# Kernel tuning notes

Hardware: AMD Instinct MI355X
Metric: run time of the kernel (lower is better)

Reference implementation:

```python
import jax, jax.numpy as jnp
import numpy as np

N, F_IN, H, C, E = 100000, 128, 64, 40, 1600000
NEG_SLOPE = 0.2


def setup_inputs() -> dict:
    key = jax.random.key(0)
    ks = jax.random.split(key, 12)
    s = 0.1
    return {
        "x": jax.random.normal(ks[0], (N, F_IN), jnp.float32),
        "edge_index": jax.random.randint(ks[1], (2, E), 0, N, jnp.int32),
        "W1": jax.random.normal(ks[2], (F_IN, H), jnp.float32) * s,
        "a_src1": jax.random.normal(ks[3], (H,), jnp.float32) * s,
        "a_dst1": jax.random.normal(ks[4], (H,), jnp.float32) * s,
        "b1": jnp.zeros((H,), jnp.float32),
        "W2": jax.random.normal(ks[5], (H, H), jnp.float32) * s,
        "a_src2": jax.random.normal(ks[6], (H,), jnp.float32) * s,
        "a_dst2": jax.random.normal(ks[7], (H,), jnp.float32) * s,
        "b2": jnp.zeros((H,), jnp.float32),
        "Wl": jax.random.normal(ks[8], (H, C), jnp.float32) * s,
        "bl": jnp.zeros((C,), jnp.float32),
    }


def gat_conv(x, src, dst, W, a_src, a_dst, b):
    # PyG GATConv, heads=1, self-loops already appended to (src, dst)
    h = x @ W                                   # [N, H]
    alpha_s = h @ a_src                         # [N]
    alpha_d = h @ a_dst                         # [N]
    e = jax.nn.leaky_relu(alpha_s[src] + alpha_d[dst], NEG_SLOPE)  # [E]
    # segment softmax over incoming edges of each target node
    m = jax.ops.segment_max(e, dst, num_segments=x.shape[0])
    ex = jnp.exp(e - m[dst])
    denom = jax.ops.segment_sum(ex, dst, num_segments=x.shape[0])
    w = ex / (denom[dst] + 1e-16)               # [E]
    out = jax.ops.segment_sum(h[src] * w[:, None], dst, num_segments=x.shape[0])
    return out + b


def reference(x, edge_index, W1, a_src1, a_dst1, b1, W2, a_src2, a_dst2, b2, Wl, bl):
    n = x.shape[0]
    loops = jnp.arange(n, dtype=edge_index.dtype)
    src = jnp.concatenate([edge_index[0], loops])
    dst = jnp.concatenate([edge_index[1], loops])
    h = gat_conv(x, src, dst, W1, a_src1, a_dst1, b1)
    h = jax.nn.relu(h)  # dropout p=0 -> identity
    h = gat_conv(h, src, dst, W2, a_src2, a_dst2, b2)
    logits = h @ Wl + bl
    return jax.nn.log_softmax(logits, axis=-1)
```

## Files before the change

kernel.cpp:

```cpp
#include <hip/hip_runtime.h>
#include <math.h>


#define NEG_SLOPE 0.2f
#define NEG_BIG -3.0e38f

#define BSHIFT 9
#define BSIZE 512
#define BCAP 12288
#define EPB 4096

typedef __bf16 bf16x8 __attribute__((ext_vector_type(8)));
typedef __bf16 bf16x4 __attribute__((ext_vector_type(4)));
typedef float f32x4 __attribute__((ext_vector_type(4)));

__device__ __forceinline__ float lrelu(float x) {
    return x >= 0.f ? x : NEG_SLOPE * x;
}

__device__ __forceinline__ int wave_incl_scan(int v, int lane) {
#pragma unroll
    for (int d = 1; d < 64; d <<= 1) {
        int t = __shfl_up(v, d, 64);
        if (lane >= d) v += t;
    }
    return v;
}


__global__ __launch_bounds__(256) void fused_scatter_gemm(
        const int* __restrict__ src, const int* __restrict__ dst,
        int* __restrict__ bucketCount, unsigned* __restrict__ ebuf, int E, int SB,
        const float* __restrict__ X, const float* __restrict__ W,
        const float* __restrict__ a_src, const float* __restrict__ a_dst,
        __bf16* __restrict__ Hout, float* __restrict__ as_, float* __restrict__ ad_,
        int N, int nTiles) {
    constexpr int K = 128;
    __shared__ __bf16 Whi[64][K + 8];
    __shared__ __bf16 Wlo[64][K + 8];
    __shared__ int hist[256], base[256];

    if (blockIdx.x < (unsigned)SB) {
        const int t = threadIdx.x;
        hist[t] = 0;
        __syncthreads();
        const int e0 = blockIdx.x * EPB;
        const int e1 = min(e0 + EPB, E);
        int rr[EPB / 256];
#pragma unroll
        for (int i = 0; i < EPB / 256; ++i) {
            int e = e0 + i * 256 + t;
            if (e < e1) rr[i] = atomicAdd(&hist[dst[e] >> BSHIFT], 1);
        }
        __syncthreads();
        if (hist[t] > 0) base[t] = atomicAdd(&bucketCount[t], hist[t]);
        __syncthreads();
#pragma unroll
        for (int i = 0; i < EPB / 256; ++i) {
            int e = e0 + i * 256 + t;
            if (e < e1) {
                int d = dst[e];
                int b = d >> BSHIFT;
                ebuf[(size_t)b * BCAP + base[b] + rr[i]] =
                    ((unsigned)src[e] << BSHIFT) | (unsigned)(d & (BSIZE - 1));
            }
        }
        return;
    }

    const int gbid = blockIdx.x - SB;
    for (int idx = threadIdx.x; idx < K * 64; idx += 256) {
        int k = idx >> 6, n = idx & 63;
        float w = W[idx];
        __bf16 hi = (__bf16)w;
        Whi[n][k] = hi;
        Wlo[n][k] = (__bf16)(w - (float)hi);
    }
    __syncthreads();

    const int lane  = threadIdx.x & 63;
    const int wave  = threadIdx.x >> 6;
    const int row16 = lane & 15;
    const int quad  = lane >> 4;

    float asv[4], adv[4];
#pragma unroll
    for (int t = 0; t < 4; ++t) {
        asv[t] = a_src[t * 16 + row16];
        adv[t] = a_dst[t * 16 + row16];
    }

    for (int tile = gbid; tile < nTiles; tile += 1024) {
        const int nbase = tile * 64;
        int gn = nbase + wave * 16 + row16;
        if (gn >= N) gn = N - 1;
        const float* __restrict__ xp = X + (size_t)gn * K + quad * 8;

        float4 xv[K / 16];
#pragma unroll
        for (int c = 0; c < K / 32; ++c) {
            xv[2 * c]     = *(const float4*)(xp + c * 32);
            xv[2 * c + 1] = *(const float4*)(xp + c * 32 + 4);
        }

        f32x4 acc[4] = {{0.f, 0.f, 0.f, 0.f}, {0.f, 0.f, 0.f, 0.f},
                        {0.f, 0.f, 0.f, 0.f}, {0.f, 0.f, 0.f, 0.f}};
#pragma unroll
        for (int kc = 0; kc < K; kc += 32) {
            float xs[8];
            *(float4*)&xs[0] = xv[kc / 16];
            *(float4*)&xs[4] = xv[kc / 16 + 1];
            bf16x8 ahi, alo;
#pragma unroll
            for (int j = 0; j < 8; ++j) {
                __bf16 hi = (__bf16)xs[j];
                ahi[j] = hi;
                alo[j] = (__bf16)(xs[j] - (float)hi);
            }
#pragma unroll
            for (int t = 0; t < 4; ++t) {
                bf16x8 bhi = *(const bf16x8*)&Whi[t * 16 + row16][kc + quad * 8];
                bf16x8 blo = *(const bf16x8*)&Wlo[t * 16 + row16][kc + quad * 8];
                acc[t] = __builtin_amdgcn_mfma_f32_16x16x32_bf16(ahi, bhi, acc[t], 0, 0, 0);
                acc[t] = __builtin_amdgcn_mfma_f32_16x16x32_bf16(ahi, blo, acc[t], 0, 0, 0);
                acc[t] = __builtin_amdgcn_mfma_f32_16x16x32_bf16(alo, bhi, acc[t], 0, 0, 0);
            }
        }

        float ps[4] = {0.f, 0.f, 0.f, 0.f};
        float pd[4] = {0.f, 0.f, 0.f, 0.f};
#pragma unroll
        for (int t = 0; t < 4; ++t) {
#pragma unroll
            for (int r = 0; r < 4; ++r) {
                int gm = nbase + wave * 16 + quad * 4 + r;
                if (gm < N) Hout[(size_t)gm * 64 + t * 16 + row16] = (__bf16)acc[t][r];
                ps[r] = fmaf(acc[t][r], asv[t], ps[r]);
                pd[r] = fmaf(acc[t][r], adv[t], pd[r]);
            }
        }
#pragma unroll
        for (int r = 0; r < 4; ++r) {
#pragma unroll
            for (int d = 1; d < 16; d <<= 1) {
                ps[r] += __shfl_xor(ps[r], d, 64);
                pd[r] += __shfl_xor(pd[r], d, 64);
            }
        }
        if (row16 == 0) {
#pragma unroll
            for (int r = 0; r < 4; ++r) {
                int gm = nbase + wave * 16 + quad * 4 + r;
                if (gm < N) { as_[gm] = ps[r]; ad_[gm] = pd[r]; }
            }
        }
    }
}


__global__ __launch_bounds__(512) void bucket_csr(const unsigned* __restrict__ ebuf,
                                                  const int* __restrict__ bucketCount,
                                                  int* __restrict__ offs,
                                                  int* __restrict__ csr, int N, int E) {
    __shared__ int hist[512], excls[512], wsum[8];
    const int b = blockIdx.x;
    const int t = threadIdx.x;
    const int lane = t & 63;
    const int w = t >> 6;

    int v = (t < 256 && t < b) ? bucketCount[t] : 0;
#pragma unroll
    for (int d = 32; d; d >>= 1) v += __shfl_xor(v, d, 64);
    if (lane == 0) wsum[w] = v;
    hist[t] = 0;
    __syncthreads();
    int gbase = 0;
#pragma unroll
    for (int i = 0; i < 8; ++i) gbase += wsum[i];
    const int cnt = bucketCount[b];
    if (b == 0 && t == 0) offs[N] = E;

    const unsigned* __restrict__ eb = ebuf + (size_t)b * BCAP;
    int rr[BCAP / 512];
#pragma unroll
    for (int i = 0; i < BCAP / 512; ++i) {
        int idx = i * 512 + t;
        if (idx < cnt) rr[i] = atomicAdd(&hist[eb[idx] & (BSIZE - 1)], 1);
    }
    __syncthreads();

    int hv = hist[t];
    int incl = wave_incl_scan(hv, lane);
    if (lane == 63) wsum[w] = incl;
    __syncthreads();
    int prefix = 0;
    for (int i = 0; i < 8; ++i) prefix += (i < w) ? wsum[i] : 0;
    int excl = incl - hv + prefix;
    int n = b * BSIZE + t;
    if (n < N) offs[n] = gbase + excl;
    excls[t] = excl;
    __syncthreads();

#pragma unroll
    for (int i = 0; i < BCAP / 512; ++i) {
        int idx = i * 512 + t;
        if (idx < cnt) {
            unsigned rec = eb[idx];
            csr[gbase + excls[rec & (BSIZE - 1)] + rr[i]] = (int)(rec >> BSHIFT);
        }
    }
}


__global__ __launch_bounds__(256) void gemm_mfma2(const __bf16* __restrict__ X,
                                                  const float* __restrict__ W,
                                                  const float* __restrict__ a_src,
                                                  const float* __restrict__ a_dst,
                                                  __bf16* __restrict__ Hout,
                                                  float* __restrict__ as_,
                                                  float* __restrict__ ad_,
                                                  int N, int nTiles) {
    constexpr int K = 64;
    __shared__ __bf16 Whi[64][K + 8];
    __shared__ __bf16 Wlo[64][K + 8];
    for (int idx = threadIdx.x; idx < K * 64; idx += 256) {
        int k = idx >> 6, n = idx & 63;
        float w = W[idx];
        __bf16 hi = (__bf16)w;
        Whi[n][k] = hi;
        Wlo[n][k] = (__bf16)(w - (float)hi);
    }
    __syncthreads();

    const int lane  = threadIdx.x & 63;
    const int wave  = threadIdx.x >> 6;
    const int row16 = lane & 15;
    const int quad  = lane >> 4;

    float asv[4], adv[4];
#pragma unroll
    for (int t = 0; t < 4; ++t) {
        asv[t] = a_src[t * 16 + row16];
        adv[t] = a_dst[t * 16 + row16];
    }

    for (int tile = blockIdx.x; tile < nTiles; tile += gridDim.x) {
        const int nbase = tile * 64;
        int gn = nbase + wave * 16 + row16;
        if (gn >= N) gn = N - 1;
        const __bf16* __restrict__ xp = X + (size_t)gn * K + quad * 8;
        bf16x8 a0 = *(const bf16x8*)(xp);
        bf16x8 a1 = *(const bf16x8*)(xp + 32);

        f32x4 acc[4] = {{0.f, 0.f, 0.f, 0.f}, {0.f, 0.f, 0.f, 0.f},
                        {0.f, 0.f, 0.f, 0.f}, {0.f, 0.f, 0.f, 0.f}};
#pragma unroll
        for (int kc = 0; kc < K; kc += 32) {
            bf16x8 a = (kc == 0) ? a0 : a1;
#pragma unroll
            for (int t = 0; t < 4; ++t) {
                bf16x8 bhi = *(const bf16x8*)&Whi[t * 16 + row16][kc + quad * 8];
                bf16x8 blo = *(const bf16x8*)&Wlo[t * 16 + row16][kc + quad * 8];
                acc[t] = __builtin_amdgcn_mfma_f32_16x16x32_bf16(a, bhi, acc[t], 0, 0, 0);
                acc[t] = __builtin_amdgcn_mfma_f32_16x16x32_bf16(a, blo, acc[t], 0, 0, 0);
            }
        }

        float ps[4] = {0.f, 0.f, 0.f, 0.f};
        float pd[4] = {0.f, 0.f, 0.f, 0.f};
#pragma unroll
        for (int t = 0; t < 4; ++t) {
#pragma unroll
            for (int r = 0; r < 4; ++r) {
                int gm = nbase + wave * 16 + quad * 4 + r;
                if (gm < N) Hout[(size_t)gm * 64 + t * 16 + row16] = (__bf16)acc[t][r];
                ps[r] = fmaf(acc[t][r], asv[t], ps[r]);
                pd[r] = fmaf(acc[t][r], adv[t], pd[r]);
            }
        }
#pragma unroll
        for (int r = 0; r < 4; ++r) {
#pragma unroll
            for (int d = 1; d < 16; d <<= 1) {
                ps[r] += __shfl_xor(ps[r], d, 64);
                pd[r] += __shfl_xor(pd[r], d, 64);
            }
        }
        if (row16 == 0) {
#pragma unroll
            for (int r = 0; r < 4; ++r) {
                int gm = nbase + wave * 16 + quad * 4 + r;
                if (gm < N) { as_[gm] = ps[r]; ad_[gm] = pd[r]; }
            }
        }
    }
}


__global__ __launch_bounds__(256) void gat_agg(const __bf16* __restrict__ h,
                                               const float* __restrict__ as_,
                                               const float* __restrict__ ad_,
                                               const float* __restrict__ bias,
                                               const int* __restrict__ offs,
                                               const int* __restrict__ csr,
                                               __bf16* __restrict__ out,
                                               int N, int do_relu) {
    int gtid = blockIdx.x * blockDim.x + threadIdx.x;
    int n = __builtin_amdgcn_readfirstlane(gtid >> 6);
    if (n >= N) return;
    const int lane = threadIdx.x & 63;
    const int g  = lane >> 4;
    const int fl = lane & 15;

    int beg = offs[n], end = offs[n + 1];
    float adn = ad_[n];
    float p_self = __expf(lrelu(as_[n] + adn));

    float den = p_self;
    float ax, ay, az, aw;
    {
        bf16x4 t = *(const bf16x4*)(h + (size_t)n * 64 + fl * 4);
        float m0 = (g == 0) ? p_self : 0.f;
        ax = m0 * (float)t[0];
        ay = m0 * (float)t[1];
        az = m0 * (float)t[2];
        aw = m0 * (float)t[3];
    }

    for (int c0 = beg; c0 < end; c0 += 64) {
        int cnt = end - c0;
        if (cnt > 64) cnt = 64;
        int   s_l = (lane < cnt) ? csr[c0 + lane] : 0;
        float p_l = (lane < cnt) ? __expf(lrelu(as_[s_l] + adn)) : 0.f;
        float csum = p_l;
#pragma unroll
        for (int d = 32; d; d >>= 1) csum += __shfl_xor(csum, d, 64);
        den += csum;

        int rounds = (cnt + 3) >> 2;
        for (int r = 0; r < rounds; r += 4) {
            int j0 = (r + 0) * 4 + g, j1 = (r + 1) * 4 + g;
            int j2 = (r + 2) * 4 + g, j3 = (r + 3) * 4 + g;
            float w0 = __shfl(p_l, j0, 64), w1 = __shfl(p_l, j1, 64);
            float w2 = __shfl(p_l, j2, 64), w3 = __shfl(p_l, j3, 64);
            int s0 = __shfl(s_l, j0, 64), s1 = __shfl(s_l, j1, 64);
            int s2 = __shfl(s_l, j2, 64), s3 = __shfl(s_l, j3, 64);
            bf16x4 h0 = *(const bf16x4*)(h + (size_t)s0 * 64 + fl * 4);
            bf16x4 h1 = *(const bf16x4*)(h + (size_t)s1 * 64 + fl * 4);
            bf16x4 h2 = *(const bf16x4*)(h + (size_t)s2 * 64 + fl * 4);
            bf16x4 h3 = *(const bf16x4*)(h + (size_t)s3 * 64 + fl * 4);
            ax = fmaf(w0, (float)h0[0], ax); ay = fmaf(w0, (float)h0[1], ay);
            az = fmaf(w0, (float)h0[2], az); aw = fmaf(w0, (float)h0[3], aw);
            ax = fmaf(w1, (float)h1[0], ax); ay = fmaf(w1, (float)h1[1], ay);
            az = fmaf(w1, (float)h1[2], az); aw = fmaf(w1, (float)h1[3], aw);
            ax = fmaf(w2, (float)h2[0], ax); ay = fmaf(w2, (float)h2[1], ay);
            az = fmaf(w2, (float)h2[2], az); aw = fmaf(w2, (float)h2[3], aw);
            ax = fmaf(w3, (float)h3[0], ax); ay = fmaf(w3, (float)h3[1], ay);
            az = fmaf(w3, (float)h3[2], az); aw = fmaf(w3, (float)h3[3], aw);
        }
    }

#pragma unroll
    for (int d = 16; d <= 32; d <<= 1) {
        ax += __shfl_xor(ax, d, 64);
        ay += __shfl_xor(ay, d, 64);
        az += __shfl_xor(az, d, 64);
        aw += __shfl_xor(aw, d, 64);
    }
    if (g == 0) {
        float inv = 1.f / (den + 1e-16f);
        const float4 b4 = *(const float4*)(bias + fl * 4);
        bf16x4 ov;
        float o0 = fmaf(ax, inv, b4.x);
        float o1 = fmaf(ay, inv, b4.y);
        float o2 = fmaf(az, inv, b4.z);
        float o3 = fmaf(aw, inv, b4.w);
        if (do_relu) {
            o0 = fmaxf(o0, 0.f); o1 = fmaxf(o1, 0.f);
            o2 = fmaxf(o2, 0.f); o3 = fmaxf(o3, 0.f);
        }
        ov[0] = (__bf16)o0; ov[1] = (__bf16)o1;
        ov[2] = (__bf16)o2; ov[3] = (__bf16)o3;
        *(bf16x4*)(out + (size_t)n * 64 + fl * 4) = ov;
    }
}


__global__ __launch_bounds__(256) void final_lsm(const __bf16* __restrict__ h,
                                                 const float* __restrict__ Wl,
                                                 const float* __restrict__ bl,
                                                 float* __restrict__ out,
                                                 int N, int nTiles) {
    __shared__ __bf16 Whi[48][72];
    __shared__ __bf16 Wlo[48][72];
    __shared__ float bls[48];
    for (int idx = threadIdx.x; idx < 48 * 64; idx += 256) {
        int c = idx >> 6, k = idx & 63;
        float w = (c < 40) ? Wl[k * 40 + c] : 0.f;
        __bf16 hi = (__bf16)w;
        Whi[c][k] = hi;
        Wlo[c][k] = (__bf16)(w - (float)hi);
    }
    if (threadIdx.x < 48) bls[threadIdx.x] = (threadIdx.x < 40) ? bl[threadIdx.x] : 0.f;
    __syncthreads();

    const int lane  = threadIdx.x & 63;
    const int wave  = threadIdx.x >> 6;
    const int col16 = lane & 15;
    const int quad  = lane >> 4;

    for (int tile = blockIdx.x; tile < nTiles; tile += gridDim.x) {
        const int nbase = tile * 64;
        int gn = nbase + wave * 16 + col16;
        if (gn >= N) gn = N - 1;
        const __bf16* __restrict__ xp = h + (size_t)gn * 64 + quad * 8;
        bf16x8 a0 = *(const bf16x8*)(xp);
        bf16x8 a1 = *(const bf16x8*)(xp + 32);

        f32x4 acc[3] = {{0.f, 0.f, 0.f, 0.f}, {0.f, 0.f, 0.f, 0.f},
                        {0.f, 0.f, 0.f, 0.f}};
#pragma unroll
        for (int kc = 0; kc < 64; kc += 32) {
            bf16x8 a = (kc == 0) ? a0 : a1;
#pragma unroll
            for (int t = 0; t < 3; ++t) {
                bf16x8 bhi = *(const bf16x8*)&Whi[t * 16 + col16][kc + quad * 8];
                bf16x8 blo = *(const bf16x8*)&Wlo[t * 16 + col16][kc + quad * 8];
                acc[t] = __builtin_amdgcn_mfma_f32_16x16x32_bf16(a, bhi, acc[t], 0, 0, 0);
                acc[t] = __builtin_amdgcn_mfma_f32_16x16x32_bf16(a, blo, acc[t], 0, 0, 0);
            }
        }

#pragma unroll
        for (int r = 0; r < 4; ++r) {
            int gm = nbase + wave * 16 + quad * 4 + r;
            float l0 = acc[0][r] + bls[col16];
            float l1 = acc[1][r] + bls[16 + col16];
            float l2 = (col16 < 8) ? (acc[2][r] + bls[32 + col16]) : NEG_BIG;
            float mx = fmaxf(fmaxf(l0, l1), l2);
#pragma unroll
            for (int d = 1; d < 16; d <<= 1) mx = fmaxf(mx, __shfl_xor(mx, d, 64));
            float s = __expf(l0 - mx) + __expf(l1 - mx) +
                      ((col16 < 8) ? __expf(l2 - mx) : 0.f);
#pragma unroll
            for (int d = 1; d < 16; d <<= 1) s += __shfl_xor(s, d, 64);
            float lse = mx + __logf(s);
            if (gm < N) {
                out[(size_t)gm * 40 + col16]      = l0 - lse;
                out[(size_t)gm * 40 + 16 + col16] = l1 - lse;
                if (col16 < 8) out[(size_t)gm * 40 + 32 + col16] = l2 - lse;
            }
        }
    }
}


extern "C" void kernel_launch(void* const* d_in, const int* in_sizes, int n_in,
                              void* d_out, int out_size, void* d_ws, size_t ws_size,
                              hipStream_t stream) {
    const float* x      = (const float*)d_in[0];
    const int*   ei     = (const int*)d_in[1];
    const float* W1     = (const float*)d_in[2];
    const float* a_src1 = (const float*)d_in[3];
    const float* a_dst1 = (const float*)d_in[4];
    const float* b1     = (const float*)d_in[5];
    const float* W2     = (const float*)d_in[6];
    const float* a_src2 = (const float*)d_in[7];
    const float* a_dst2 = (const float*)d_in[8];
    const float* b2     = (const float*)d_in[9];
    const float* Wl     = (const float*)d_in[10];
    const float* bl     = (const float*)d_in[11];

    const int N = in_sizes[0] / 128;
    const int E = in_sizes[1] / 2;
    const int* src = ei;
    const int* dst = ei + E;
    const int nbuck = (N + BSIZE - 1) >> BSHIFT;
    const int SB = (E + EPB - 1) / EPB;

    char* p = (char*)d_ws;
    auto alloc = [&](size_t bytes) -> void* {
        void* r = (void*)p;
        p += (bytes + 255) & ~(size_t)255;
        return r;
    };
    int*      offs        = (int*)alloc((size_t)(N + 1) * 4);
    int*      bucketCount = (int*)alloc(256 * 4);
    unsigned* ebuf        = (unsigned*)alloc((size_t)nbuck * BCAP * 4);
    int*      csr         = (int*)alloc((size_t)E * 4);
    __bf16*   hbf         = (__bf16*)alloc((size_t)N * 64 * 2);
    __bf16*   habg        = (__bf16*)alloc((size_t)N * 64 * 2);
    float*    as_         = (float*)alloc((size_t)N * 4);
    float*    ad_         = (float*)alloc((size_t)N * 4);

    hipMemsetAsync(bucketCount, 0, 256 * 4, stream);

    const int nTiles = (N + 63) / 64;
    int aggBlocks = (N * 64 + 255) / 256;

    fused_scatter_gemm<<<SB + 1024, 256, 0, stream>>>(
        src, dst, bucketCount, ebuf, E, SB,
        x, W1, a_src1, a_dst1, hbf, as_, ad_, N, nTiles);
    bucket_csr<<<nbuck, 512, 0, stream>>>(ebuf, bucketCount, offs, csr, N, E);
    gat_agg<<<aggBlocks, 256, 0, stream>>>(hbf, as_, ad_, b1, offs, csr, habg, N, 1);
    gemm_mfma2<<<1024, 256, 0, stream>>>(habg, W2, a_src2, a_dst2, hbf, as_, ad_, N, nTiles);
    gat_agg<<<aggBlocks, 256, 0, stream>>>(hbf, as_, ad_, b2, offs, csr, habg, N, 0);
    final_lsm<<<nTiles, 256, 0, stream>>>(habg, Wl, bl, (float*)d_out, N, nTiles);
}
```

Before: 284.1 us.

## Interleave scatter and GEMM blocks, shrink edge chunks, pad bucket counters, widen CSR blocks

Cuts edges per scatter block from 4096 to 1024, so there are about four times as many scatter blocks. When there are enough of them, scatter and GEMM blocks are interleaved by block index so both kinds of work run on the GPU at the same time. Global bucket counters are padded to a 16-int stride, which spreads atomics across separate cache lines. The bucket_csr kernel now uses 1024 threads per block instead of 512, halving the per-thread loop count. The cost is many more global atomics on the counters and more scatter-block launches.

```diff
diff --git a/kernel.cpp b/kernel.cpp
--- a/kernel.cpp
+++ b/kernel.cpp
@@ -8,7 +8,8 @@
 #define BSHIFT 9
 #define BSIZE 512
 #define BCAP 12288
-#define EPB 4096
+#define EPB 1024
+#define BCSTR 16
 
 typedef __bf16 bf16x8 __attribute__((ext_vector_type(8)));
 typedef __bf16 bf16x4 __attribute__((ext_vector_type(4)));
@@ -40,11 +41,27 @@
     __shared__ __bf16 Wlo[64][K + 8];
     __shared__ int hist[256], base[256];
 
-    if (blockIdx.x < (unsigned)SB) {
+    const int bid = blockIdx.x;
+    bool isScatter;
+    int sid = 0, gbid = 0;
+    if (SB >= 1024) {
+        if (bid < 2048) {
+            isScatter = (bid & 1);
+            if (isScatter) sid = bid >> 1; else gbid = bid >> 1;
+        } else {
+            isScatter = true;
+            sid = bid - 1024;
+        }
+    } else {
+        isScatter = bid < SB;
+        if (isScatter) sid = bid; else gbid = bid - SB;
+    }
+
+    if (isScatter) {
         const int t = threadIdx.x;
         hist[t] = 0;
         __syncthreads();
-        const int e0 = blockIdx.x * EPB;
+        const int e0 = sid * EPB;
         const int e1 = min(e0 + EPB, E);
         int rr[EPB / 256];
 #pragma unroll
@@ -53,7 +70,7 @@
             if (e < e1) rr[i] = atomicAdd(&hist[dst[e] >> BSHIFT], 1);
         }
         __syncthreads();
-        if (hist[t] > 0) base[t] = atomicAdd(&bucketCount[t], hist[t]);
+        if (hist[t] > 0) base[t] = atomicAdd(&bucketCount[t * BCSTR], hist[t]);
         __syncthreads();
 #pragma unroll
         for (int i = 0; i < EPB / 256; ++i) {
@@ -68,7 +85,6 @@
         return;
     }
 
-    const int gbid = blockIdx.x - SB;
     for (int idx = threadIdx.x; idx < K * 64; idx += 256) {
         int k = idx >> 6, n = idx & 63;
         float w = W[idx];
@@ -158,52 +174,55 @@
 }
 
 
-__global__ __launch_bounds__(512) void bucket_csr(const unsigned* __restrict__ ebuf,
-                                                  const int* __restrict__ bucketCount,
-                                                  int* __restrict__ offs,
-                                                  int* __restrict__ csr, int N, int E) {
-    __shared__ int hist[512], excls[512], wsum[8];
+__global__ __launch_bounds__(1024) void bucket_csr(const unsigned* __restrict__ ebuf,
+                                                   const int* __restrict__ bucketCount,
+                                                   int* __restrict__ offs,
+                                                   int* __restrict__ csr, int N, int E) {
+    __shared__ int hist[512], excls[512], wsum[16];
     const int b = blockIdx.x;
     const int t = threadIdx.x;
     const int lane = t & 63;
     const int w = t >> 6;
 
-    int v = (t < 256 && t < b) ? bucketCount[t] : 0;
+    int v = (t < 256 && t < b) ? bucketCount[t * BCSTR] : 0;
 #pragma unroll
     for (int d = 32; d; d >>= 1) v += __shfl_xor(v, d, 64);
     if (lane == 0) wsum[w] = v;
-    hist[t] = 0;
+    if (t < 512) hist[t] = 0;
     __syncthreads();
     int gbase = 0;
 #pragma unroll
-    for (int i = 0; i < 8; ++i) gbase += wsum[i];
-    const int cnt = bucketCount[b];
+    for (int i = 0; i < 16; ++i) gbase += wsum[i];
+    const int cnt = bucketCount[b * BCSTR];
     if (b == 0 && t == 0) offs[N] = E;
 
     const unsigned* __restrict__ eb = ebuf + (size_t)b * BCAP;
-    int rr[BCAP / 512];
-#pragma unroll
-    for (int i = 0; i < BCAP / 512; ++i) {
-        int idx = i * 512 + t;
+    int rr[BCAP / 1024];
+#pragma unroll
+    for (int i = 0; i < BCAP / 1024; ++i) {
+        int idx = i * 1024 + t;
         if (idx < cnt) rr[i] = atomicAdd(&hist[eb[idx] & (BSIZE - 1)], 1);
     }
     __syncthreads();
 
-    int hv = hist[t];
+    int hv = (t < 512) ? hist[t] : 0;
     int incl = wave_incl_scan(hv, lane);
-    if (lane == 63) wsum[w] = incl;
-    __syncthreads();
-    int prefix = 0;
-    for (int i = 0; i < 8; ++i) prefix += (i < w) ? wsum[i] : 0;
-    int excl = incl - hv + prefix;
-    int n = b * BSIZE + t;
-    if (n < N) offs[n] = gbase + excl;
-    excls[t] = excl;
-    __syncthreads();
-
-#pragma unroll
-    for (int i = 0; i < BCAP / 512; ++i) {
-        int idx = i * 512 + t;
+    if (lane == 63 && w < 8) wsum[w] = incl;
+    __syncthreads();
+    if (t < 512) {
+        int prefix = 0;
+#pragma unroll
+        for (int i = 0; i < 8; ++i) prefix += (i < w) ? wsum[i] : 0;
+        int excl = incl - hv + prefix;
+        int n = b * BSIZE + t;
+        if (n < N) offs[n] = gbase + excl;
+        excls[t] = excl;
+    }
+    __syncthreads();
+
+#pragma unroll
+    for (int i = 0; i < BCAP / 1024; ++i) {
+        int idx = i * 1024 + t;
         if (idx < cnt) {
             unsigned rec = eb[idx];
             csr[gbase + excls[rec & (BSIZE - 1)] + rr[i]] = (int)(rec >> BSHIFT);
@@ -485,7 +504,7 @@
         return r;
     };
     int*      offs        = (int*)alloc((size_t)(N + 1) * 4);
-    int*      bucketCount = (int*)alloc(256 * 4);
+    int*      bucketCount = (int*)alloc(256 * BCSTR * 4);
     unsigned* ebuf        = (unsigned*)alloc((size_t)nbuck * BCAP * 4);
     int*      csr         = (int*)alloc((size_t)E * 4);
     __bf16*   hbf         = (__bf16*)alloc((size_t)N * 64 * 2);
@@ -493,7 +512,7 @@
     float*    as_         = (float*)alloc((size_t)N * 4);
     float*    ad_         = (float*)alloc((size_t)N * 4);
 
-    hipMemsetAsync(bucketCount, 0, 256 * 4, stream);
+    hipMemsetAsync(bucketCount, 0, 256 * BCSTR * 4, stream);
 
     const int nTiles = (N + 63) / 64;
     int aggBlocks = (N * 64 + 255) / 256;
@@ -501,7 +520,7 @@
     fused_scatter_gemm<<<SB + 1024, 256, 0, stream>>>(
         src, dst, bucketCount, ebuf, E, SB,
         x, W1, a_src1, a_dst1, hbf, as_, ad_, N, nTiles);
-    bucket_csr<<<nbuck, 512, 0, stream>>>(ebuf, bucketCount, offs, csr, N, E);
+    bucket_csr<<<nbuck, 1024, 0, stream>>>(ebuf, bucketCount, offs, csr, N, E);
     gat_agg<<<aggBlocks, 256, 0, stream>>>(hbf, as_, ad_, b1, offs, csr, habg, N, 1);
     gemm_mfma2<<<1024, 256, 0, stream>>>(habg, W2, a_src2, a_dst2, hbf, as_, ad_, N, nTiles);
     gat_agg<<<aggBlocks, 256, 0, stream>>>(hbf, as_, ad_, b2, offs, csr, habg, N, 0);
```

Result: no change. 285.9 us (+0.6%).

## Build CSR via global degree count and atomic-cursor scatter instead of bucket sort

Applied to the files above, without the earlier changes.

Replaces the two-pass bucketed counting sort (scatter into per-bucket staging buffer, then per-bucket local sort) with a global per-node degree histogram, a per-bucket prefix scan to produce offsets and cursors, and a separate edge scatter kernel that places each source via atomicAdd on the destination's cursor. This removes the intermediate ebuf staging traffic but adds global atomics per edge (two passes) and an extra kernel launch. Edge order within each node's neighbour list becomes nondeterministic, which can change float summation order.

```diff
diff --git a/kernel.cpp b/kernel.cpp
--- a/kernel.cpp
+++ b/kernel.cpp
@@ -7,8 +7,7 @@
 
 #define BSHIFT 9
 #define BSIZE 512
-#define BCAP 12288
-#define EPB 4096
+#define CEPB 8192
 
 typedef __bf16 bf16x8 __attribute__((ext_vector_type(8)));
 typedef __bf16 bf16x4 __attribute__((ext_vector_type(4)));
@@ -28,9 +27,9 @@
 }
 
 
-__global__ __launch_bounds__(256) void fused_scatter_gemm(
-        const int* __restrict__ src, const int* __restrict__ dst,
-        int* __restrict__ bucketCount, unsigned* __restrict__ ebuf, int E, int SB,
+__global__ __launch_bounds__(256) void fused_count_gemm(
+        const int* __restrict__ dst, int* __restrict__ deg,
+        int* __restrict__ bucketCount, int E, int CB,
         const float* __restrict__ X, const float* __restrict__ W,
         const float* __restrict__ a_src, const float* __restrict__ a_dst,
         __bf16* __restrict__ Hout, float* __restrict__ as_, float* __restrict__ ad_,
@@ -38,37 +37,25 @@
     constexpr int K = 128;
     __shared__ __bf16 Whi[64][K + 8];
     __shared__ __bf16 Wlo[64][K + 8];
-    __shared__ int hist[256], base[256];
-
-    if (blockIdx.x < (unsigned)SB) {
+    __shared__ int hist[256];
+
+    if (blockIdx.x < (unsigned)CB) {
         const int t = threadIdx.x;
         hist[t] = 0;
         __syncthreads();
-        const int e0 = blockIdx.x * EPB;
-        const int e1 = min(e0 + EPB, E);
-        int rr[EPB / 256];
-#pragma unroll
-        for (int i = 0; i < EPB / 256; ++i) {
-            int e = e0 + i * 256 + t;
-            if (e < e1) rr[i] = atomicAdd(&hist[dst[e] >> BSHIFT], 1);
+        const int e0 = blockIdx.x * CEPB;
+        const int e1 = min(e0 + CEPB, E);
+        for (int e = e0 + t; e < e1; e += 256) {
+            int d = dst[e];
+            atomicAdd(&deg[d], 1);
+            atomicAdd(&hist[d >> BSHIFT], 1);
         }
         __syncthreads();
-        if (hist[t] > 0) base[t] = atomicAdd(&bucketCount[t], hist[t]);
-        __syncthreads();
-#pragma unroll
-        for (int i = 0; i < EPB / 256; ++i) {
-            int e = e0 + i * 256 + t;
-            if (e < e1) {
-                int d = dst[e];
-                int b = d >> BSHIFT;
-                ebuf[(size_t)b * BCAP + base[b] + rr[i]] =
-                    ((unsigned)src[e] << BSHIFT) | (unsigned)(d & (BSIZE - 1));
-            }
-        }
+        if (hist[t] > 0) atomicAdd(&bucketCount[t], hist[t]);
         return;
     }
 
-    const int gbid = blockIdx.x - SB;
+    const int gbid = blockIdx.x - CB;
     for (int idx = threadIdx.x; idx < K * 64; idx += 256) {
         int k = idx >> 6, n = idx & 63;
         float w = W[idx];
@@ -158,11 +145,12 @@
 }
 
 
-__global__ __launch_bounds__(512) void bucket_csr(const unsigned* __restrict__ ebuf,
-                                                  const int* __restrict__ bucketCount,
-                                                  int* __restrict__ offs,
-                                                  int* __restrict__ csr, int N, int E) {
-    __shared__ int hist[512], excls[512], wsum[8];
+__global__ __launch_bounds__(512) void node_offs(const int* __restrict__ deg,
+                                                 const int* __restrict__ bucketCount,
+                                                 int* __restrict__ offs,
+                                                 int* __restrict__ cursor,
+                                                 int N, int E) {
+    __shared__ int gsum[8], wsum[8];
     const int b = blockIdx.x;
     const int t = threadIdx.x;
     const int lane = t & 63;
@@ -171,44 +159,40 @@
     int v = (t < 256 && t < b) ? bucketCount[t] : 0;
 #pragma unroll
     for (int d = 32; d; d >>= 1) v += __shfl_xor(v, d, 64);
-    if (lane == 0) wsum[w] = v;
-    hist[t] = 0;
+    if (lane == 0) gsum[w] = v;
     __syncthreads();
     int gbase = 0;
 #pragma unroll
-    for (int i = 0; i < 8; ++i) gbase += wsum[i];
-    const int cnt = bucketCount[b];
-    if (b == 0 && t == 0) offs[N] = E;
-
-    const unsigned* __restrict__ eb = ebuf + (size_t)b * BCAP;
-    int rr[BCAP / 512];
-#pragma unroll
-    for (int i = 0; i < BCAP / 512; ++i) {
-        int idx = i * 512 + t;
-        if (idx < cnt) rr[i] = atomicAdd(&hist[eb[idx] & (BSIZE - 1)], 1);
-    }
-    __syncthreads();
-
-    int hv = hist[t];
-    int incl = wave_incl_scan(hv, lane);
+    for (int i = 0; i < 8; ++i) gbase += gsum[i];
+
+    const int n = b * BSIZE + t;
+    const int dv = (n < N) ? deg[n] : 0;
+    int incl = wave_incl_scan(dv, lane);
     if (lane == 63) wsum[w] = incl;
     __syncthreads();
     int prefix = 0;
+#pragma unroll
     for (int i = 0; i < 8; ++i) prefix += (i < w) ? wsum[i] : 0;
-    int excl = incl - hv + prefix;
-    int n = b * BSIZE + t;
-    if (n < N) offs[n] = gbase + excl;
-    excls[t] = excl;
-    __syncthreads();
-
-#pragma unroll
-    for (int i = 0; i < BCAP / 512; ++i) {
-        int idx = i * 512 + t;
-        if (idx < cnt) {
-            unsigned rec = eb[idx];
-            csr[gbase + excls[rec & (BSIZE - 1)] + rr[i]] = (int)(rec >> BSHIFT);
-        }
-    }
+    int excl = incl - dv + prefix;
+    if (n < N) {
+        int o = gbase + excl;
+        offs[n] = o;
+        cursor[n] = o;
+    }
+    if (b == 0 && t == 0) offs[N] = E;
+}
+
+
+__global__ __launch_bounds__(256) void edge_scatter(const int* __restrict__ src,
+                                                    const int* __restrict__ dst,
+                                                    int* __restrict__ cursor,
+                                                    int* __restrict__ csr, int E) {
+    int e = blockIdx.x * 256 + threadIdx.x;
+    if (e >= E) return;
+    int s = src[e];
+    int d = dst[e];
+    int pos = atomicAdd(&cursor[d], 1);
+    csr[pos] = s;
 }
 
 
@@ -476,7 +460,7 @@
     const int* src = ei;
     const int* dst = ei + E;
     const int nbuck = (N + BSIZE - 1) >> BSHIFT;
-    const int SB = (E + EPB - 1) / EPB;
+    const int CB = (E + CEPB - 1) / CEPB;
 
     char* p = (char*)d_ws;
     auto alloc = [&](size_t bytes) -> void* {
@@ -485,23 +469,26 @@
         return r;
     };
     int*      offs        = (int*)alloc((size_t)(N + 1) * 4);
+    int*      deg         = (int*)alloc((size_t)N * 4);
     int*      bucketCount = (int*)alloc(256 * 4);
-    unsigned* ebuf        = (unsigned*)alloc((size_t)nbuck * BCAP * 4);
+    int*      cursor      = (int*)alloc((size_t)N * 4);
     int*      csr         = (int*)alloc((size_t)E * 4);
     __bf16*   hbf         = (__bf16*)alloc((size_t)N * 64 * 2);
     __bf16*   habg        = (__bf16*)alloc((size_t)N * 64 * 2);
     float*    as_         = (float*)alloc((size_t)N * 4);
     float*    ad_         = (float*)alloc((size_t)N * 4);
 
-    hipMemsetAsync(bucketCount, 0, 256 * 4, stream);
+    size_t degPad = ((size_t)N * 4 + 255) & ~(size_t)255;
+    hipMemsetAsync(deg, 0, degPad + 256 * 4, stream);
 
     const int nTiles = (N + 63) / 64;
     int aggBlocks = (N * 64 + 255) / 256;
 
-    fused_scatter_gemm<<<SB + 1024, 256, 0, stream>>>(
-        src, dst, bucketCount, ebuf, E, SB,
+    fused_count_gemm<<<CB + 1024, 256, 0, stream>>>(
+        dst, deg, bucketCount, E, CB,
         x, W1, a_src1, a_dst1, hbf, as_, ad_, N, nTiles);
-    bucket_csr<<<nbuck, 512, 0, stream>>>(ebuf, bucketCount, offs, csr, N, E);
+    node_offs<<<nbuck, 512, 0, stream>>>(deg, bucketCount, offs, cursor, N, E);
+    edge_scatter<<<(E + 255) / 256, 256, 0, stream>>>(src, dst, cursor, csr, E);
     gat_agg<<<aggBlocks, 256, 0, stream>>>(hbf, as_, ad_, b1, offs, csr, habg, N, 1);
     gemm_mfma2<<<1024, 256, 0, stream>>>(habg, W2, a_src2, a_dst2, hbf, as_, ad_, N, nTiles);
     gat_agg<<<aggBlocks, 256, 0, stream>>>(hbf, as_, ad_, b2, offs, csr, habg, N, 0);
```

Result: slower. 424.0 us (+49.2%).

## Replace atomic bucket reservation with per-chunk fixed-capacity slots and separate scan

Applied to the files above, without the earlier changes.

The edge-bucketing pass no longer reserves space in each bucket with global atomics and a second barrier. Instead each chunk of 8192 edges writes its records into a fixed-capacity slot per (bucket, chunk) and stores a per-chunk histogram. A one-block scan kernel computes bucket starts, and a 1024-thread fill kernel walks the chunk slots to build the CSR. This removes contention on the bucket counters, at the cost of an extra kernel launch and a hard per-slot capacity of 112 edges that could overflow on skewed inputs.

```diff
diff --git a/kernel.cpp b/kernel.cpp
--- a/kernel.cpp
+++ b/kernel.cpp
@@ -7,8 +7,9 @@
 
 #define BSHIFT 9
 #define BSIZE 512
-#define BCAP 12288
-#define EPB 4096
+#define CEPB 8192
+#define ECAP 112
+#define CBPAD 256
 
 typedef __bf16 bf16x8 __attribute__((ext_vector_type(8)));
 typedef __bf16 bf16x4 __attribute__((ext_vector_type(4)));
@@ -28,9 +29,10 @@
 }
 
 
-__global__ __launch_bounds__(256) void fused_scatter_gemm(
+__global__ __launch_bounds__(256) void fused_hist_gemm(
         const int* __restrict__ src, const int* __restrict__ dst,
-        int* __restrict__ bucketCount, unsigned* __restrict__ ebuf, int E, int SB,
+        int* __restrict__ bucketCount, int* __restrict__ blockHist,
+        unsigned* __restrict__ ebuf, int E, int CB,
         const float* __restrict__ X, const float* __restrict__ W,
         const float* __restrict__ a_src, const float* __restrict__ a_dst,
         __bf16* __restrict__ Hout, float* __restrict__ as_, float* __restrict__ ad_,
@@ -38,37 +40,39 @@
     constexpr int K = 128;
     __shared__ __bf16 Whi[64][K + 8];
     __shared__ __bf16 Wlo[64][K + 8];
-    __shared__ int hist[256], base[256];
-
-    if (blockIdx.x < (unsigned)SB) {
+    __shared__ int hist[256];
+
+    if (blockIdx.x < (unsigned)CB) {
         const int t = threadIdx.x;
         hist[t] = 0;
         __syncthreads();
-        const int e0 = blockIdx.x * EPB;
-        const int e1 = min(e0 + EPB, E);
-        int rr[EPB / 256];
-#pragma unroll
-        for (int i = 0; i < EPB / 256; ++i) {
+        const int c = blockIdx.x;
+        const int e0 = c * CEPB;
+        const int e1 = min(e0 + CEPB, E);
+        int rr[CEPB / 256];
+#pragma unroll
+        for (int i = 0; i < CEPB / 256; ++i) {
             int e = e0 + i * 256 + t;
             if (e < e1) rr[i] = atomicAdd(&hist[dst[e] >> BSHIFT], 1);
         }
         __syncthreads();
-        if (hist[t] > 0) base[t] = atomicAdd(&bucketCount[t], hist[t]);
-        __syncthreads();
-#pragma unroll
-        for (int i = 0; i < EPB / 256; ++i) {
+        int hv = hist[t];
+        blockHist[t * CBPAD + c] = hv;
+        if (hv > 0) atomicAdd(&bucketCount[t], hv);
+#pragma unroll
+        for (int i = 0; i < CEPB / 256; ++i) {
             int e = e0 + i * 256 + t;
             if (e < e1) {
                 int d = dst[e];
                 int b = d >> BSHIFT;
-                ebuf[(size_t)b * BCAP + base[b] + rr[i]] =
+                ebuf[((size_t)b * CB + c) * ECAP + rr[i]] =
                     ((unsigned)src[e] << BSHIFT) | (unsigned)(d & (BSIZE - 1));
             }
         }
         return;
     }
 
-    const int gbid = blockIdx.x - SB;
+    const int gbid = blockIdx.x - CB;
     for (int idx = threadIdx.x; idx < K * 64; idx += 256) {
         int k = idx >> 6, n = idx & 63;
         float w = W[idx];
@@ -158,55 +162,88 @@
 }
 
 
-__global__ __launch_bounds__(512) void bucket_csr(const unsigned* __restrict__ ebuf,
-                                                  const int* __restrict__ bucketCount,
-                                                  int* __restrict__ offs,
-                                                  int* __restrict__ csr, int N, int E) {
-    __shared__ int hist[512], excls[512], wsum[8];
+__global__ __launch_bounds__(256) void bucket_scan(const int* __restrict__ bucketCount,
+                                                   int* __restrict__ bucketStart,
+                                                   int* __restrict__ offs,
+                                                   int N, int E) {
+    __shared__ int wsum[4];
+    const int t = threadIdx.x;
+    const int lane = t & 63;
+    const int w = t >> 6;
+    int v = bucketCount[t];
+    int incl = wave_incl_scan(v, lane);
+    if (lane == 63) wsum[w] = incl;
+    __syncthreads();
+    int pre = 0;
+#pragma unroll
+    for (int i = 0; i < 4; ++i) pre += (i < w) ? wsum[i] : 0;
+    bucketStart[t] = incl - v + pre;
+    if (t == 0) offs[N] = E;
+}
+
+
+__global__ __launch_bounds__(1024) void bucket_fill(const unsigned* __restrict__ ebuf,
+                                                    const int* __restrict__ blockHist,
+                                                    const int* __restrict__ bucketStart,
+                                                    int* __restrict__ offs,
+                                                    int* __restrict__ csr,
+                                                    int N, int CB) {
+    __shared__ int hist[512], excls[512], bhist_s[256], wsum[16];
     const int b = blockIdx.x;
     const int t = threadIdx.x;
     const int lane = t & 63;
     const int w = t >> 6;
-
-    int v = (t < 256 && t < b) ? bucketCount[t] : 0;
-#pragma unroll
-    for (int d = 32; d; d >>= 1) v += __shfl_xor(v, d, 64);
-    if (lane == 0) wsum[w] = v;
-    hist[t] = 0;
-    __syncthreads();
-    int gbase = 0;
-#pragma unroll
-    for (int i = 0; i < 8; ++i) gbase += wsum[i];
-    const int cnt = bucketCount[b];
-    if (b == 0 && t == 0) offs[N] = E;
-
-    const unsigned* __restrict__ eb = ebuf + (size_t)b * BCAP;
-    int rr[BCAP / 512];
-#pragma unroll
-    for (int i = 0; i < BCAP / 512; ++i) {
-        int idx = i * 512 + t;
-        if (idx < cnt) rr[i] = atomicAdd(&hist[eb[idx] & (BSIZE - 1)], 1);
-    }
-    __syncthreads();
-
-    int hv = hist[t];
+    const int gbase = bucketStart[b];
+
+    if (t < 512) hist[t] = 0;
+    if (t < 256) bhist_s[t] = blockHist[b * CBPAD + t];
+    __syncthreads();
+
+    int rr[32];
+#pragma unroll
+    for (int ci = 0; ci < 16; ++ci) {
+        int c = w + ci * 16;
+        int cnt = (c < CB) ? bhist_s[c] : 0;
+        const unsigned* __restrict__ ep = ebuf + ((size_t)b * CB + c) * ECAP;
+#pragma unroll
+        for (int ri = 0; ri < 2; ++ri) {
+            int idx = ri * 64 + lane;
+            if (idx < cnt) {
+                unsigned rec = ep[idx];
+                rr[ci * 2 + ri] = atomicAdd(&hist[rec & (BSIZE - 1)], 1);
+            }
+        }
+    }
+    __syncthreads();
+
+    int hv = (t < 512) ? hist[t] : 0;
     int incl = wave_incl_scan(hv, lane);
-    if (lane == 63) wsum[w] = incl;
-    __syncthreads();
-    int prefix = 0;
-    for (int i = 0; i < 8; ++i) prefix += (i < w) ? wsum[i] : 0;
-    int excl = incl - hv + prefix;
-    int n = b * BSIZE + t;
-    if (n < N) offs[n] = gbase + excl;
-    excls[t] = excl;
-    __syncthreads();
-
-#pragma unroll
-    for (int i = 0; i < BCAP / 512; ++i) {
-        int idx = i * 512 + t;
-        if (idx < cnt) {
-            unsigned rec = eb[idx];
-            csr[gbase + excls[rec & (BSIZE - 1)] + rr[i]] = (int)(rec >> BSHIFT);
+    if (lane == 63 && w < 8) wsum[w] = incl;
+    __syncthreads();
+    if (t < 512) {
+        int pre = 0;
+#pragma unroll
+        for (int i = 0; i < 8; ++i) pre += (i < w) ? wsum[i] : 0;
+        int excl = incl - hv + pre;
+        int n = b * BSIZE + t;
+        if (n < N) offs[n] = gbase + excl;
+        excls[t] = excl;
+    }
+    __syncthreads();
+
+#pragma unroll
+    for (int ci = 0; ci < 16; ++ci) {
+        int c = w + ci * 16;
+        int cnt = (c < CB) ? bhist_s[c] : 0;
+        const unsigned* __restrict__ ep = ebuf + ((size_t)b * CB + c) * ECAP;
+#pragma unroll
+        for (int ri = 0; ri < 2; ++ri) {
+            int idx = ri * 64 + lane;
+            if (idx < cnt) {
+                unsigned rec = ep[idx];
+                csr[gbase + excls[rec & (BSIZE - 1)] + rr[ci * 2 + ri]] =
+                    (int)(rec >> BSHIFT);
+            }
         }
     }
 }
@@ -476,7 +513,7 @@
     const int* src = ei;
     const int* dst = ei + E;
     const int nbuck = (N + BSIZE - 1) >> BSHIFT;
-    const int SB = (E + EPB - 1) / EPB;
+    const int CB = (E + CEPB - 1) / CEPB;
 
     char* p = (char*)d_ws;
     auto alloc = [&](size_t bytes) -> void* {
@@ -486,7 +523,9 @@
     };
     int*      offs        = (int*)alloc((size_t)(N + 1) * 4);
     int*      bucketCount = (int*)alloc(256 * 4);
-    unsigned* ebuf        = (unsigned*)alloc((size_t)nbuck * BCAP * 4);
+    int*      bucketStart = (int*)alloc(256 * 4);
+    int*      blockHist   = (int*)alloc(256 * CBPAD * 4);
+    unsigned* ebuf        = (unsigned*)alloc((size_t)nbuck * CB * ECAP * 4);
     int*      csr         = (int*)alloc((size_t)E * 4);
     __bf16*   hbf         = (__bf16*)alloc((size_t)N * 64 * 2);
     __bf16*   habg        = (__bf16*)alloc((size_t)N * 64 * 2);
@@ -498,10 +537,12 @@
     const int nTiles = (N + 63) / 64;
     int aggBlocks = (N * 64 + 255) / 256;
 
-    fused_scatter_gemm<<<SB + 1024, 256, 0, stream>>>(
-        src, dst, bucketCount, ebuf, E, SB,
+    fused_hist_gemm<<<CB + 1024, 256, 0, stream>>>(
+        src, dst, bucketCount, blockHist, ebuf, E, CB,
         x, W1, a_src1, a_dst1, hbf, as_, ad_, N, nTiles);
-    bucket_csr<<<nbuck, 512, 0, stream>>>(ebuf, bucketCount, offs, csr, N, E);
+    bucket_scan<<<1, 256, 0, stream>>>(bucketCount, bucketStart, offs, N, E);
+    bucket_fill<<<nbuck, 1024, 0, stream>>>(ebuf, blockHist, bucketStart,
+                                            offs, csr, N, CB);
     gat_agg<<<aggBlocks, 256, 0, stream>>>(hbf, as_, ad_, b1, offs, csr, habg, N, 1);
     gemm_mfma2<<<1024, 256, 0, stream>>>(habg, W2, a_src2, a_dst2, hbf, as_, ad_, N, nTiles);
     gat_agg<<<aggBlocks, 256, 0, stream>>>(hbf, as_, ad_, b2, offs, csr, habg, N, 0);
```

After: 286.7 us. Within noise of the previous version (+0.9%).
